# Optimization experiments

Hardware: AMD Instinct MI355X
Metric: run time of the kernel (lower is better)

## Reference

```python
import jax, jax.numpy as jnp
import numpy as np
import math

B, S, D = 2, 1024, 1024
H = 16
HD = D // H
E = 8
DFF = 4096
EPS = 1e-5


def _ln(x, g, b):
    m = jnp.mean(x, axis=-1, keepdims=True)
    v = jnp.mean((x - m) ** 2, axis=-1, keepdims=True)
    return (x - m) / jnp.sqrt(v + EPS) * g + b


def setup_inputs() -> dict:
    key = jax.random.key(0)
    ks = jax.random.split(key, 16)
    s = 0.02
    inp = {
        'src': jax.random.normal(ks[0], (B, S, D), jnp.float32),
        'qw': jax.random.normal(ks[1], (D, D), jnp.float32) * s,
        'kw': jax.random.normal(ks[2], (D, D), jnp.float32) * s,
        'vw': jax.random.normal(ks[3], (D, D), jnp.float32) * s,
        'ow': jax.random.normal(ks[4], (D, D), jnp.float32) * s,
        'gate_w': jax.random.normal(ks[5], (D, D), jnp.float32) * s,
        'gate_b': jax.random.normal(ks[6], (D,), jnp.float32) * s,
        'scale_w': jax.random.normal(ks[7], (H, HD), jnp.float32) * s,
        'n1_g': jnp.ones((D,), jnp.float32),
        'n1_b': jnp.zeros((D,), jnp.float32),
        'n2_g': jnp.ones((D,), jnp.float32),
        'n2_b': jnp.zeros((D,), jnp.float32),
        'moe_gate_w': jax.random.normal(ks[8], (D, E), jnp.float32) * s,
        'moe_gate_b': jnp.zeros((E,), jnp.float32),
        'w1': jax.random.normal(ks[9], (E, D, DFF), jnp.float32) * s,
        'b1': jnp.zeros((E, DFF), jnp.float32),
        'ln_g': jnp.ones((E, DFF), jnp.float32),
        'ln_b': jnp.zeros((E, DFF), jnp.float32),
        'w2': jax.random.normal(ks[10], (E, DFF, D), jnp.float32) * s,
        'b2': jnp.zeros((E, D), jnp.float32),
        'res_scale': jnp.ones((E,), jnp.float32),
    }
    return inp


def _forward(src, qw, kw, vw, ow, gate_w, gate_b, scale_w, n1_g, n1_b, n2_g, n2_b,
             moe_gate_w, moe_gate_b, w1, b1, ln_g, ln_b, w2, b2, res_scale):
    # ---- MemoAttention (non-flash path, eval: no dropout, no mask) ----
    q = (src @ qw).reshape(B, S, H, HD).transpose(0, 2, 1, 3)  # [B,H,S,HD]
    k = (src @ kw).reshape(B, S, H, HD).transpose(0, 2, 1, 3)
    v = (src @ vw).reshape(B, S, H, HD).transpose(0, 2, 1, 3)
    scores = jnp.einsum('bhqd,bhkd->bhqk', q, k) / math.sqrt(HD)
    # dynamic per-(head,query) scale gate
    scale = jax.nn.sigmoid(jnp.einsum('bhsd,hd->bhs', q, scale_w)) * 2.0
    scores = scores * scale[..., None]
    attn = jax.nn.softmax(scores, axis=-1)
    out = jnp.einsum('bhqk,bhkd->bhqd', attn, v)
    out = out.transpose(0, 2, 1, 3).reshape(B, S, D)
    gate = jax.nn.sigmoid(out @ gate_w + gate_b)
    attn_out = (out * gate) @ ow

    x = _ln(src + attn_out, n1_g, n1_b)

    # ---- MoE FFN (top-2 routing; eval: no gate noise; capacity never exceeded) ----
    xf = x.reshape(-1, D)                      # [T, D]
    T = xf.shape[0]
    logits = xf @ moe_gate_w + moe_gate_b      # [T, E]
    top_v, top_i = jax.lax.top_k(logits, 2)
    # NB: original sums BOTH top-k softmax weights per token (== 1.0), and the
    wsum = jnp.sum(jax.nn.softmax(top_v, axis=-1), axis=-1)   # [T] (== 1)
    e_sel = jnp.max(top_i, axis=-1)                           # [T]
    # dense per-expert FFN on all tokens, then per-token select (masked compute)
    h = jnp.einsum('td,edf->etf', xf, w1) + b1[:, None, :]    # [E,T,DFF]
    h = _ln(h, ln_g[:, None, :], ln_b[:, None, :])
    h = jax.nn.gelu(h, approximate=False)                     # torch nn.GELU (erf)
    y = jnp.einsum('etf,efd->etd', h, w2) + b2[:, None, :]    # [E,T,D]
    y = y * res_scale[:, None, None] + xf[None]
    sel = jnp.take_along_axis(y, e_sel[None, :, None], axis=0)[0]  # [T,D]
    moe_out = (sel * wsum[:, None]).reshape(B, S, D)

    return _ln(x + moe_out, n2_g, n2_b)


def reference(src, qw, kw, vw, ow, gate_w, gate_b, scale_w, n1_g, n1_b, n2_g, n2_b,
              moe_gate_w, moe_gate_b, w1, b1, ln_g, ln_b, w2, b2, res_scale):
    return _forward(src, qw, kw, vw, ow, gate_w, gate_b, scale_w, n1_g, n1_b,
                    n2_g, n2_b, moe_gate_w, moe_gate_b, w1, b1, ln_g, ln_b,
                    w2, b2, res_scale)
```

## Files before the change

kernel.cpp:

```cpp
#include <hip/hip_runtime.h>
#include <math.h>

#define TOK    2048
#define DMODEL 1024
#define NHEAD  16
#define HDIM   64
#define NEXP   8
#define DFFN   4096

typedef unsigned short u16;
typedef __attribute__((ext_vector_type(8))) short short8;
typedef __attribute__((ext_vector_type(4))) float floatx4;

__device__ __forceinline__ float sigmoidf_(float x) { return 1.f / (1.f + expf(-x)); }

__device__ __forceinline__ u16 f2bf(float f) {
  union { float f; unsigned u; } v; v.f = f;
  unsigned r = v.u + 0x7FFFu + ((v.u >> 16) & 1u);
  return (u16)(r >> 16);
}
__device__ __forceinline__ float bf2f(u16 h) {
  union { unsigned u; float f; } v; v.u = ((unsigned)h) << 16; return v.f;
}

__device__ __forceinline__ void gload16(const void* g, void* l) {
  __builtin_amdgcn_global_load_lds((const __attribute__((address_space(1))) void*)g,
                                   (__attribute__((address_space(3))) void*)l, 16, 0, 0);
}

__device__ __forceinline__ float blockReduceSum256(float val) {
  __shared__ float ws_[4];
  #pragma unroll
  for (int off = 32; off; off >>= 1) val += __shfl_down(val, off);
  int lane = threadIdx.x & 63, w = threadIdx.x >> 6;
  if (lane == 0) ws_[w] = val;
  __syncthreads();
  float r = ws_[0] + ws_[1] + ws_[2] + ws_[3];
  __syncthreads();
  return r;
}

__global__ __launch_bounds__(256) void split_kernel(
    const float* __restrict__ X, u16* __restrict__ Hi, u16* __restrict__ Lo) {
  const int i = blockIdx.x * 256 + threadIdx.x;
  const float4 v = ((const float4*)X)[i];
  const float f[4] = {v.x, v.y, v.z, v.w};
  union { u16 s[4]; uint2 u; } h, l;
  #pragma unroll
  for (int j = 0; j < 4; ++j) {
    h.s[j] = f2bf(f[j]);
    l.s[j] = f2bf(f[j] - bf2f(h.s[j]));
  }
  ((uint2*)Hi)[i] = h.u;
  ((uint2*)Lo)[i] = l.u;
}

template<bool LO>
__global__ __launch_bounds__(256) void wt_conv_kernel(
    const float* __restrict__ W, u16* __restrict__ Whi, u16* __restrict__ Wlo,
    int K, int N) {
  const size_t z = blockIdx.z;
  W   += z * (size_t)K * N;
  Whi += z * (size_t)K * N;
  if (LO) Wlo += z * (size_t)K * N;
  __shared__ float tile[32][33];
  const int n0 = blockIdx.x * 32, k0 = blockIdx.y * 32;
  const int r = threadIdx.x >> 3, c4 = (threadIdx.x & 7) * 4;
  const float4 v = *(const float4*)&W[(size_t)(k0 + r) * N + n0 + c4];
  tile[r][c4+0] = v.x; tile[r][c4+1] = v.y; tile[r][c4+2] = v.z; tile[r][c4+3] = v.w;
  __syncthreads();
  union { u16 s[4]; uint2 u; } h, l;
  #pragma unroll
  for (int j = 0; j < 4; ++j) {
    const float f = tile[c4 + j][r];
    h.s[j] = f2bf(f);
    if (LO) l.s[j] = f2bf(f - bf2f(h.s[j]));
  }
  *(uint2*)&Whi[(size_t)(n0 + r) * K + k0 + c4] = h.u;
  if (LO) *(uint2*)&Wlo[(size_t)(n0 + r) * K + k0 + c4] = l.u;
}

template<int EPI>
__global__ __launch_bounds__(256, 2) void gemm_split_kernel(
    const u16* __restrict__ Ahi, const u16* __restrict__ Alo,
    const u16* __restrict__ Whi, const u16* __restrict__ Wlo,
    const float* __restrict__ bias, const float* __restrict__ mul,
    float* __restrict__ Cf, u16* __restrict__ Chi, u16* __restrict__ Clo,
    int M, int N, int K) {
  __shared__ u16 Ah[128*64], Al[128*64], Bh[128*64], Bl[128*64];
  const int tid = threadIdx.x;
  const int lane = tid & 63, wave = tid >> 6;
  const int row0 = blockIdx.y * 128, col0 = blockIdx.x * 128;
  const int wm = (wave & 1) * 64, wn = (wave >> 1) * 64;
  const int mr = tid >> 3;
  const int ksrc = (tid & 7) ^ ((tid >> 3) & 7);
  const floatx4 zero = {0.f, 0.f, 0.f, 0.f};
  floatx4 acc[4][4];
  #pragma unroll
  for (int i = 0; i < 4; ++i)
    #pragma unroll
    for (int j = 0; j < 4; ++j) acc[i][j] = zero;

  for (int k0 = 0; k0 < K; k0 += 64) {
    __syncthreads();
    #pragma unroll
    for (int p = 0; p < 4; ++p) {
      const int m = p * 32 + mr;
      const size_t ga = (size_t)(row0 + m) * K + (k0 + ksrc * 8);
      const size_t gb = (size_t)(col0 + m) * K + (k0 + ksrc * 8);
      const size_t off = (size_t)(p * 256 + wave * 64) * 16;
      gload16(Ahi + ga, (char*)Ah + off);
      gload16(Alo + ga, (char*)Al + off);
      gload16(Whi + gb, (char*)Bh + off);
      gload16(Wlo + gb, (char*)Bl + off);
    }
    __syncthreads();
    #pragma unroll
    for (int kk = 0; kk < 2; ++kk) {
      short8 ah[4], al[4], bh[4], bl[4];
      #pragma unroll
      for (int i = 0; i < 4; ++i) {
        const int ml = wm + i * 16 + (lane & 15);
        const int cm = (kk * 4 + (lane >> 4)) ^ (ml & 7);
        ah[i] = *(const short8*)&Ah[ml * 64 + cm * 8];
        al[i] = *(const short8*)&Al[ml * 64 + cm * 8];
        const int nl = wn + i * 16 + (lane & 15);
        const int cn = (kk * 4 + (lane >> 4)) ^ (nl & 7);
        bh[i] = *(const short8*)&Bh[nl * 64 + cn * 8];
        bl[i] = *(const short8*)&Bl[nl * 64 + cn * 8];
      }
      #pragma unroll
      for (int i = 0; i < 4; ++i)
        #pragma unroll
        for (int j = 0; j < 4; ++j) {
          acc[i][j] = __builtin_amdgcn_mfma_f32_16x16x32_bf16(ah[i], bh[j], acc[i][j], 0, 0, 0);
          acc[i][j] = __builtin_amdgcn_mfma_f32_16x16x32_bf16(al[i], bh[j], acc[i][j], 0, 0, 0);
          acc[i][j] = __builtin_amdgcn_mfma_f32_16x16x32_bf16(ah[i], bl[j], acc[i][j], 0, 0, 0);
        }
    }
  }
  const int cl = lane & 15, quad = lane >> 4;
  #pragma unroll
  for (int i = 0; i < 4; ++i)
    #pragma unroll
    for (int j = 0; j < 4; ++j) {
      const int col = col0 + wn + j * 16 + cl;
      #pragma unroll
      for (int r = 0; r < 4; ++r) {
        const int row = row0 + wm + i * 16 + quad * 4 + r;
        const float v = acc[i][j][r];
        if (EPI == 0) {
          Cf[(size_t)row * N + col] = v;
        } else if (EPI == 1) {
          const float s = sigmoidf_(v + bias[col]);
          const float g = s * mul[(size_t)row * N + col];
          const u16 hh = f2bf(g);
          Chi[(size_t)row * N + col] = hh;
          Clo[(size_t)row * N + col] = f2bf(g - bf2f(hh));
        } else {
          const u16 hh = f2bf(v);
          Chi[(size_t)row * N + col] = hh;
          Clo[(size_t)row * N + col] = f2bf(v - bf2f(hh));
        }
      }
    }
}

template<int EPI>
__global__ __launch_bounds__(256, 2) void gemm_moe_kernel(
    const u16* __restrict__ A, const u16* __restrict__ Wt,
    const float* __restrict__ bias, const float* __restrict__ rsc,
    const float* __restrict__ Xres,
    const int* __restrict__ perm, const int* __restrict__ offs,
    const int* __restrict__ counts,
    u16* __restrict__ Hout, float* __restrict__ Yout,
    int N, int K, int e_base) {
  const int ez = blockIdx.z, e = e_base + ez;
  const int ne = counts[e];
  const int tm = blockIdx.y;
  if (tm * 128 >= ne) return;
  __shared__ u16 As_[128*64], Bs_[128*64];
  __shared__ int toks[128];
  const int tid = threadIdx.x;
  if (tid < 128) {
    const int idx = tm * 128 + tid;
    toks[tid] = perm[offs[e] + (idx < ne ? idx : 0)];
  }
  __syncthreads();
  const int lane = tid & 63, wave = tid >> 6;
  const int wm = (wave & 1) * 64, wn = (wave >> 1) * 64;
  const int mr = tid >> 3;
  const int ksrc = (tid & 7) ^ ((tid >> 3) & 7);
  size_t abase[4];
  #pragma unroll
  for (int p = 0; p < 4; ++p) abase[p] = (size_t)toks[p * 32 + mr] * K;
  const u16* We = Wt + (size_t)ez * N * K;
  const int col0 = blockIdx.x * 128;
  const floatx4 zero = {0.f, 0.f, 0.f, 0.f};
  floatx4 acc[4][4];
  #pragma unroll
  for (int i = 0; i < 4; ++i)
    #pragma unroll
    for (int j = 0; j < 4; ++j) acc[i][j] = zero;

  for (int k0 = 0; k0 < K; k0 += 64) {
    __syncthreads();
    #pragma unroll
    for (int p = 0; p < 4; ++p) {
      const size_t off = (size_t)(p * 256 + wave * 64) * 16;
      gload16(A + abase[p] + (k0 + ksrc * 8), (char*)As_ + off);
      gload16(We + (size_t)(col0 + p * 32 + mr) * K + (k0 + ksrc * 8), (char*)Bs_ + off);
    }
    __syncthreads();
    #pragma unroll
    for (int kk = 0; kk < 2; ++kk) {
      short8 a[4], b[4];
      #pragma unroll
      for (int i = 0; i < 4; ++i) {
        const int ml = wm + i * 16 + (lane & 15);
        const int cm = (kk * 4 + (lane >> 4)) ^ (ml & 7);
        a[i] = *(const short8*)&As_[ml * 64 + cm * 8];
        const int nl = wn + i * 16 + (lane & 15);
        const int cn = (kk * 4 + (lane >> 4)) ^ (nl & 7);
        b[i] = *(const short8*)&Bs_[nl * 64 + cn * 8];
      }
      #pragma unroll
      for (int i = 0; i < 4; ++i)
        #pragma unroll
        for (int j = 0; j < 4; ++j)
          acc[i][j] = __builtin_amdgcn_mfma_f32_16x16x32_bf16(a[i], b[j], acc[i][j], 0, 0, 0);
    }
  }
  const int cl = lane & 15, quad = lane >> 4;
  const float rse = (EPI == 1) ? rsc[e] : 0.f;
  #pragma unroll
  for (int i = 0; i < 4; ++i)
    #pragma unroll
    for (int j = 0; j < 4; ++j) {
      const int col = col0 + wn + j * 16 + cl;
      #pragma unroll
      for (int r = 0; r < 4; ++r) {
        const int rl = wm + i * 16 + quad * 4 + r;
        if (tm * 128 + rl < ne) {
          const int tok = toks[rl];
          const float v = acc[i][j][r] + bias[(size_t)e * N + col];
          if (EPI == 0) Hout[(size_t)tok * N + col] = f2bf(v);
          else          Yout[(size_t)tok * N + col] = v * rse + Xres[(size_t)tok * N + col];
        }
      }
    }
}

__global__ __launch_bounds__(256) void vt_trans_kernel(
    const u16* __restrict__ QKh, const u16* __restrict__ QKl,
    u16* __restrict__ Vth, u16* __restrict__ Vtl) {
  const int tt = blockIdx.x;
  const int bh = blockIdx.y;
  const int b = bh >> 4, h = bh & 15;
  __shared__ u16 th[64][72], tl[64][72];
  const int t = threadIdx.x;
  const int r = t >> 3, c8 = (t & 7) * 8;
  #pragma unroll
  for (int p = 0; p < 2; ++p) {
    const int tok = p * 32 + r;
    const size_t g = ((size_t)b * 1024 + tt * 64 + tok) * 3072 + 2048 + h * 64 + c8;
    *(uint4*)&th[tok][c8] = *(const uint4*)&QKh[g];
    *(uint4*)&tl[tok][c8] = *(const uint4*)&QKl[g];
  }
  __syncthreads();
  #pragma unroll
  for (int p = 0; p < 2; ++p) {
    const int d = p * 32 + r;
    union { u16 s[8]; uint4 u; } oh, ol;
    #pragma unroll
    for (int j = 0; j < 8; ++j) { oh.s[j] = th[c8 + j][d]; ol.s[j] = tl[c8 + j][d]; }
    const size_t g = ((size_t)bh * 64 + d) * 1024 + tt * 64 + c8;
    *(uint4*)&Vth[g] = oh.u;
    *(uint4*)&Vtl[g] = ol.u;
  }
}

__global__ __launch_bounds__(256, 2) void attn_mfma_kernel(
    const u16* __restrict__ QKh, const u16* __restrict__ QKl,
    const u16* __restrict__ Vth, const u16* __restrict__ Vtl,
    const float* __restrict__ scale_w,
    float* __restrict__ AOf, u16* __restrict__ AOh, u16* __restrict__ AOl) {
  const int qt = blockIdx.x, h = blockIdx.y, b = blockIdx.z;
  __shared__ u16 Kh[64*64], Kl[64*64], Vh[64*64], Vl[64*64];
  __shared__ u16 Ph[4][16*72], Pl[4][16*72];
  const int tid = threadIdx.x, lane = tid & 63, wave = tid >> 6;
  const int i15 = lane & 15, quad = lane >> 4;
  const floatx4 zero = {0.f, 0.f, 0.f, 0.f};

  short8 qh[2], ql[2];
  const size_t qrow = ((size_t)b * 1024 + qt * 64 + wave * 16 + i15) * 3072 + h * 64;
  #pragma unroll
  for (int kk = 0; kk < 2; ++kk) {
    qh[kk] = *(const short8*)&QKh[qrow + kk * 32 + quad * 8];
    ql[kk] = *(const short8*)&QKl[qrow + kk * 32 + quad * 8];
  }
  float dot = 0.f;
  #pragma unroll
  for (int kk = 0; kk < 2; ++kk)
    #pragma unroll
    for (int j = 0; j < 8; ++j) {
      const float sw = scale_w[h * 64 + kk * 32 + quad * 8 + j];
      dot += (bf2f((u16)qh[kk][j]) + bf2f((u16)ql[kk][j])) * sw;
    }
  dot += __shfl_xor(dot, 16);
  dot += __shfl_xor(dot, 32);
  const float g = 2.f * sigmoidf_(dot) * 0.125f;
  float stot[4];
  #pragma unroll
  for (int r = 0; r < 4; ++r) stot[r] = __shfl(g, (lane >> 4) * 4 + r);

  float m_r[4], l_r[4];
  floatx4 Of[4];
  #pragma unroll
  for (int r = 0; r < 4; ++r) { m_r[r] = -1e30f; l_r[r] = 0.f; }
  #pragma unroll
  for (int f = 0; f < 4; ++f) Of[f] = zero;
  u16* PhW = Ph[wave];
  u16* PlW = Pl[wave];

  const int sr = tid >> 3, sc = ((tid & 7) ^ ((tid >> 3) & 7)) * 8;
  for (int kt = 0; kt < 16; ++kt) {
    __syncthreads();
    #pragma unroll
    for (int p = 0; p < 2; ++p) {
      const int row = p * 32 + sr;
      const size_t off = (size_t)(p * 256 + wave * 64) * 16;
      const size_t kg = ((size_t)b * 1024 + kt * 64 + row) * 3072 + 1024 + h * 64 + sc;
      gload16(QKh + kg, (char*)Kh + off);
      gload16(QKl + kg, (char*)Kl + off);
      const size_t vg = ((size_t)(b * 16 + h) * 64 + row) * 1024 + kt * 64 + sc;
      gload16(Vth + vg, (char*)Vh + off);
      gload16(Vtl + vg, (char*)Vl + off);
    }
    __syncthreads();
    float pm[4][4];
    #pragma unroll
    for (int jn = 0; jn < 4; ++jn) {
      floatx4 a = zero;
      #pragma unroll
      for (int kk = 0; kk < 2; ++kk) {
        const int n = jn * 16 + i15;
        const int ch = ((kk * 4 + quad) ^ (n & 7)) * 8;
        const short8 bh = *(const short8*)&Kh[n * 64 + ch];
        const short8 bl = *(const short8*)&Kl[n * 64 + ch];
        a = __builtin_amdgcn_mfma_f32_16x16x32_bf16(qh[kk], bh, a, 0, 0, 0);
        a = __builtin_amdgcn_mfma_f32_16x16x32_bf16(ql[kk], bh, a, 0, 0, 0);
        a = __builtin_amdgcn_mfma_f32_16x16x32_bf16(qh[kk], bl, a, 0, 0, 0);
      }
      #pragma unroll
      for (int r = 0; r < 4; ++r) pm[jn][r] = a[r] * stot[r];
    }
    float alpha[4];
    #pragma unroll
    for (int r = 0; r < 4; ++r) {
      float mx = fmaxf(fmaxf(pm[0][r], pm[1][r]), fmaxf(pm[2][r], pm[3][r]));
      mx = fmaxf(mx, __shfl_xor(mx, 1));
      mx = fmaxf(mx, __shfl_xor(mx, 2));
      mx = fmaxf(mx, __shfl_xor(mx, 4));
      mx = fmaxf(mx, __shfl_xor(mx, 8));
      const float mn = fmaxf(m_r[r], mx);
      alpha[r] = expf(m_r[r] - mn);
      m_r[r] = mn;
      float rs = 0.f;
      #pragma unroll
      for (int jn = 0; jn < 4; ++jn) { pm[jn][r] = expf(pm[jn][r] - mn); rs += pm[jn][r]; }
      rs += __shfl_xor(rs, 1);
      rs += __shfl_xor(rs, 2);
      rs += __shfl_xor(rs, 4);
      rs += __shfl_xor(rs, 8);
      l_r[r] = l_r[r] * alpha[r] + rs;
    }
    #pragma unroll
    for (int f = 0; f < 4; ++f)
      #pragma unroll
      for (int r = 0; r < 4; ++r) Of[f][r] *= alpha[r];
    #pragma unroll
    for (int jn = 0; jn < 4; ++jn)
      #pragma unroll
      for (int r = 0; r < 4; ++r) {
        const int a = (quad * 4 + r) * 72 + jn * 16 + i15;
        const u16 hh = f2bf(pm[jn][r]);
        PhW[a] = hh;
        PlW[a] = f2bf(pm[jn][r] - bf2f(hh));
      }
    #pragma unroll
    for (int kk = 0; kk < 2; ++kk) {
      const short8 pah = *(const short8*)&PhW[i15 * 72 + kk * 32 + quad * 8];
      const short8 pal = *(const short8*)&PlW[i15 * 72 + kk * 32 + quad * 8];
      #pragma unroll
      for (int f = 0; f < 4; ++f) {
        const int d = f * 16 + i15;
        const int ch = ((kk * 4 + quad) ^ (d & 7)) * 8;
        const short8 vbh = *(const short8*)&Vh[d * 64 + ch];
        const short8 vbl = *(const short8*)&Vl[d * 64 + ch];
        Of[f] = __builtin_amdgcn_mfma_f32_16x16x32_bf16(pah, vbh, Of[f], 0, 0, 0);
        Of[f] = __builtin_amdgcn_mfma_f32_16x16x32_bf16(pal, vbh, Of[f], 0, 0, 0);
        Of[f] = __builtin_amdgcn_mfma_f32_16x16x32_bf16(pah, vbl, Of[f], 0, 0, 0);
      }
    }
  }
  float inv[4];
  #pragma unroll
  for (int r = 0; r < 4; ++r) inv[r] = 1.f / l_r[r];
  #pragma unroll
  for (int f = 0; f < 4; ++f)
    #pragma unroll
    for (int r = 0; r < 4; ++r) {
      const size_t row = (size_t)b * 1024 + qt * 64 + wave * 16 + quad * 4 + r;
      const int col = h * 64 + f * 16 + i15;
      const float val = Of[f][r] * inv[r];
      AOf[row * 1024 + col] = val;
      const u16 hh = f2bf(val);
      AOh[row * 1024 + col] = hh;
      AOl[row * 1024 + col] = f2bf(val - bf2f(hh));
    }
}

template<bool BF>
__global__ __launch_bounds__(256) void ln_add_kernel(
    const float* __restrict__ A, const float* __restrict__ Bp,
    const float* __restrict__ g, const float* __restrict__ beta,
    float* __restrict__ outf, u16* __restrict__ outh) {
  int t = blockIdx.x, tid = threadIdx.x;
  const float* a = A + (size_t)t * DMODEL;
  const float* b = Bp + (size_t)t * DMODEL;
  float v[4]; float s = 0.f;
  #pragma unroll
  for (int i = 0; i < 4; ++i) { int d = tid + i*256; v[i] = a[d] + b[d]; s += v[i]; }
  s = blockReduceSum256(s);
  float mean = s * (1.f/1024.f);
  float q = 0.f;
  #pragma unroll
  for (int i = 0; i < 4; ++i) { float df = v[i]-mean; q += df*df; }
  q = blockReduceSum256(q);
  float rstd = rsqrtf(q*(1.f/1024.f) + 1e-5f);
  #pragma unroll
  for (int i = 0; i < 4; ++i) {
    int d = tid + i*256;
    float val = (v[i]-mean)*rstd*g[d] + beta[d];
    outf[(size_t)t*DMODEL + d] = val;
    if (BF) outh[(size_t)t*DMODEL + d] = f2bf(val);
  }
}

__global__ __launch_bounds__(256) void moe_gate_kernel(
    const float* __restrict__ X, const float* __restrict__ gw,
    const float* __restrict__ gb, int* __restrict__ e_sel) {
  int wave = threadIdx.x >> 6, lane = threadIdx.x & 63;
  int token = blockIdx.x * 4 + wave;
  const float* x = X + (size_t)token * DMODEL;
  float acc[NEXP] = {};
  for (int d = lane; d < DMODEL; d += 64) {
    float xv = x[d];
    const float* gr = gw + (size_t)d * NEXP;
    #pragma unroll
    for (int e = 0; e < NEXP; ++e) acc[e] += xv * gr[e];
  }
  #pragma unroll
  for (int e = 0; e < NEXP; ++e) {
    #pragma unroll
    for (int off = 32; off; off >>= 1) acc[e] += __shfl_down(acc[e], off);
  }
  if (lane == 0) {
    float lg[NEXP];
    #pragma unroll
    for (int e = 0; e < NEXP; ++e) lg[e] = acc[e] + gb[e];
    int i1 = 0;
    for (int e = 1; e < NEXP; ++e) if (lg[e] > lg[i1]) i1 = e;
    int i2 = -1;
    for (int e = 0; e < NEXP; ++e) {
      if (e == i1) continue;
      if (i2 < 0 || lg[e] > lg[i2]) i2 = e;
    }
    e_sel[token] = (i1 > i2) ? i1 : i2;
  }
}

__global__ __launch_bounds__(256) void moe_group_kernel(
    const int* __restrict__ e_sel, int* __restrict__ perm,
    int* __restrict__ g_offs, int* __restrict__ g_counts) {
  __shared__ int cnt[NEXP], offs[NEXP], cur[NEXP];
  int tid = threadIdx.x;
  if (tid < NEXP) cnt[tid] = 0;
  __syncthreads();
  for (int t = tid; t < TOK; t += 256) atomicAdd(&cnt[e_sel[t]], 1);
  __syncthreads();
  if (tid == 0) {
    int run = 0;
    for (int e = 0; e < NEXP; ++e) { offs[e] = run; cur[e] = run; run += cnt[e]; }
  }
  __syncthreads();
  if (tid < NEXP) { g_offs[tid] = offs[tid]; g_counts[tid] = cnt[tid]; }
  for (int t = tid; t < TOK; t += 256) {
    int pos = atomicAdd(&cur[e_sel[t]], 1);
    perm[pos] = t;
  }
}

__global__ __launch_bounds__(256) void moe_ln_gelu_kernel(
    u16* __restrict__ H, const float* __restrict__ ln_g,
    const float* __restrict__ ln_b, const int* __restrict__ e_sel) {
  int t = blockIdx.x, tid = threadIdx.x;
  int e = e_sel[t];
  u16* h = H + (size_t)t * DFFN;
  float v[16]; float s = 0.f;
  #pragma unroll
  for (int i = 0; i < 16; ++i) { v[i] = bf2f(h[tid + i*256]); s += v[i]; }
  s = blockReduceSum256(s);
  float mean = s * (1.f/4096.f);
  float q = 0.f;
  #pragma unroll
  for (int i = 0; i < 16; ++i) { float df = v[i]-mean; q += df*df; }
  q = blockReduceSum256(q);
  float rstd = rsqrtf(q*(1.f/4096.f) + 1e-5f);
  const float* gg = ln_g + (size_t)e * DFFN;
  const float* bb = ln_b + (size_t)e * DFFN;
  #pragma unroll
  for (int i = 0; i < 16; ++i) {
    int d = tid + i*256;
    float x = (v[i]-mean)*rstd*gg[d] + bb[d];
    h[d] = f2bf(0.5f * x * (1.f + erff(x * 0.7071067811865475f)));
  }
}

extern "C" void kernel_launch(void* const* d_in, const int* in_sizes, int n_in,
                              void* d_out, int out_size, void* d_ws, size_t ws_size,
                              hipStream_t stream) {
  (void)in_sizes; (void)n_in; (void)out_size; (void)ws_size;
  const float* src    = (const float*)d_in[0];
  const float* qw     = (const float*)d_in[1];
  const float* kw     = (const float*)d_in[2];
  const float* vw     = (const float*)d_in[3];
  const float* ow     = (const float*)d_in[4];
  const float* gate_w = (const float*)d_in[5];
  const float* gate_b = (const float*)d_in[6];
  const float* scale_w= (const float*)d_in[7];
  const float* n1_g   = (const float*)d_in[8];
  const float* n1_b   = (const float*)d_in[9];
  const float* n2_g   = (const float*)d_in[10];
  const float* n2_b   = (const float*)d_in[11];
  const float* mgw    = (const float*)d_in[12];
  const float* mgb    = (const float*)d_in[13];
  const float* w1     = (const float*)d_in[14];
  const float* b1     = (const float*)d_in[15];
  const float* ln_g   = (const float*)d_in[16];
  const float* ln_b   = (const float*)d_in[17];
  const float* w2     = (const float*)d_in[18];
  const float* b2     = (const float*)d_in[19];
  const float* rs     = (const float*)d_in[20];

  char* ws = (char*)d_ws;
  const size_t MB = 1024 * 1024;
  u16*   qkv_hi = (u16*)(ws + 0*MB);
  u16*   qkv_lo = (u16*)(ws + 12*MB);
  u16*   Wt3_hi = (u16*)(ws + 24*MB);
  u16*   Wt3_lo = (u16*)(ws + 30*MB);
  u16*   Vt_hi  = (u16*)(ws + 36*MB);
  u16*   Vt_lo  = (u16*)(ws + 40*MB);
  u16*   src_hi = (u16*)(ws + 44*MB);
  u16*   src_lo = (u16*)(ws + 48*MB);
  float* ao     = (float*)(ws + 44*MB);
  u16*   ao_hi  = (u16*)(ws + 52*MB);
  u16*   ao_lo  = (u16*)(ws + 56*MB);
  u16*   gb_hi  = (u16*)(ws + 60*MB);
  u16*   gb_lo  = (u16*)(ws + 64*MB);
  float* proj   = (float*)(ws + 0*MB);
  float* x      = (float*)(ws + 8*MB);
  u16*   x_hi   = (u16*)(ws + 16*MB);
  u16*   WtA    = (u16*)(ws + 24*MB);
  u16*   h      = (u16*)(ws + 56*MB);
  float* y      = (float*)(ws + 72*MB);
  int*   e_sel  = (int*)(ws + 80*MB);
  int*   perm   = e_sel + TOK;
  int*   offs   = perm + TOK;
  int*   cnts   = offs + NEXP;

  dim3 blk(256);
  split_kernel<<<2048, blk, 0, stream>>>(src, src_hi, src_lo);

  wt_conv_kernel<true><<<dim3(32,32,1), blk, 0, stream>>>(qw, Wt3_hi, Wt3_lo, DMODEL, DMODEL);
  wt_conv_kernel<true><<<dim3(32,32,1), blk, 0, stream>>>(kw, Wt3_hi + 1024*1024, Wt3_lo + 1024*1024, DMODEL, DMODEL);
  wt_conv_kernel<true><<<dim3(32,32,1), blk, 0, stream>>>(vw, Wt3_hi + 2048*1024, Wt3_lo + 2048*1024, DMODEL, DMODEL);
  gemm_split_kernel<2><<<dim3(24,16), blk, 0, stream>>>(src_hi, src_lo, Wt3_hi, Wt3_lo,
      nullptr, nullptr, nullptr, qkv_hi, qkv_lo, TOK, 3072, DMODEL);

  vt_trans_kernel<<<dim3(16,32), blk, 0, stream>>>(qkv_hi, qkv_lo, Vt_hi, Vt_lo);
  attn_mfma_kernel<<<dim3(16, NHEAD, 2), blk, 0, stream>>>(
      qkv_hi, qkv_lo, Vt_hi, Vt_lo, scale_w, ao, ao_hi, ao_lo);

  wt_conv_kernel<true><<<dim3(32,32,1), blk, 0, stream>>>(gate_w, Wt3_hi, Wt3_lo, DMODEL, DMODEL);
  gemm_split_kernel<1><<<dim3(8,16), blk, 0, stream>>>(ao_hi, ao_lo, Wt3_hi, Wt3_lo,
      gate_b, ao, nullptr, gb_hi, gb_lo, TOK, DMODEL, DMODEL);
  wt_conv_kernel<true><<<dim3(32,32,1), blk, 0, stream>>>(ow, Wt3_hi, Wt3_lo, DMODEL, DMODEL);
  gemm_split_kernel<0><<<dim3(8,16), blk, 0, stream>>>(gb_hi, gb_lo, Wt3_hi, Wt3_lo,
      nullptr, nullptr, proj, nullptr, nullptr, TOK, DMODEL, DMODEL);

  ln_add_kernel<true><<<TOK, blk, 0, stream>>>(src, proj, n1_g, n1_b, x, x_hi);

  moe_gate_kernel<<<TOK/4, blk, 0, stream>>>(x, mgw, mgb, e_sel);
  moe_group_kernel<<<1, blk, 0, stream>>>(e_sel, perm, offs, cnts);

  for (int c = 0; c < 2; ++c) {
    wt_conv_kernel<false><<<dim3(DFFN/32, DMODEL/32, 4), blk, 0, stream>>>(
        w1 + (size_t)c*4*DMODEL*DFFN, WtA, nullptr, DMODEL, DFFN);
    gemm_moe_kernel<0><<<dim3(DFFN/128, 16, 4), blk, 0, stream>>>(
        x_hi, WtA, b1, nullptr, nullptr, perm, offs, cnts, h, nullptr, DFFN, DMODEL, c*4);
  }
  moe_ln_gelu_kernel<<<TOK, blk, 0, stream>>>(h, ln_g, ln_b, e_sel);
  for (int c = 0; c < 2; ++c) {
    wt_conv_kernel<false><<<dim3(DMODEL/32, DFFN/32, 4), blk, 0, stream>>>(
        w2 + (size_t)c*4*DFFN*DMODEL, WtA, nullptr, DFFN, DMODEL);
    gemm_moe_kernel<1><<<dim3(DMODEL/128, 16, 4), blk, 0, stream>>>(
        h, WtA, b2, rs, x, perm, offs, cnts, nullptr, y, DMODEL, DFFN, c*4);
  }
  ln_add_kernel<false><<<TOK, blk, 0, stream>>>(x, y, n2_g, n2_b, (float*)d_out, nullptr);
}
```

Before: 808.5 us.

## Halve GEMM N-tiles, split-K the MoE down-projection, fuse bias/residual into final LN

Narrows the N tile from 128 to 64 in both the split-bf16 GEMM and the MoE grouped GEMM, doubling the block count and raising the occupancy hint, so these small grids fill more compute units. The second MoE GEMM now splits K into two halves written to separate fp32 partial buffers. A new final LayerNorm kernel sums the partials and applies the bias, residual scale and residual before normalizing. This trades more redundant A-tile loads and an extra partial-buffer round trip for better parallelism on grids that were sparse because each expert receives only a few tokens.

Result: faster. 714.6 us (-11.6%).

```diff
diff --git a/kernel.cpp b/kernel.cpp
--- a/kernel.cpp
+++ b/kernel.cpp
@@ -81,58 +81,64 @@
 }
 
 template<int EPI>
-__global__ __launch_bounds__(256, 2) void gemm_split_kernel(
+__global__ __launch_bounds__(256, 3) void gemm_split_kernel(
     const u16* __restrict__ Ahi, const u16* __restrict__ Alo,
     const u16* __restrict__ Whi, const u16* __restrict__ Wlo,
     const float* __restrict__ bias, const float* __restrict__ mul,
     float* __restrict__ Cf, u16* __restrict__ Chi, u16* __restrict__ Clo,
     int M, int N, int K) {
-  __shared__ u16 Ah[128*64], Al[128*64], Bh[128*64], Bl[128*64];
+  __shared__ u16 Ah[128*64], Al[128*64], Bh[64*64], Bl[64*64];
   const int tid = threadIdx.x;
   const int lane = tid & 63, wave = tid >> 6;
-  const int row0 = blockIdx.y * 128, col0 = blockIdx.x * 128;
-  const int wm = (wave & 1) * 64, wn = (wave >> 1) * 64;
+  const int row0 = blockIdx.y * 128, col0 = blockIdx.x * 64;
+  const int wm = (wave & 1) * 64, wn = (wave >> 1) * 32;
   const int mr = tid >> 3;
   const int ksrc = (tid & 7) ^ ((tid >> 3) & 7);
   const floatx4 zero = {0.f, 0.f, 0.f, 0.f};
-  floatx4 acc[4][4];
+  floatx4 acc[4][2];
   #pragma unroll
   for (int i = 0; i < 4; ++i)
     #pragma unroll
-    for (int j = 0; j < 4; ++j) acc[i][j] = zero;
+    for (int j = 0; j < 2; ++j) acc[i][j] = zero;
 
   for (int k0 = 0; k0 < K; k0 += 64) {
     __syncthreads();
     #pragma unroll
     for (int p = 0; p < 4; ++p) {
-      const int m = p * 32 + mr;
-      const size_t ga = (size_t)(row0 + m) * K + (k0 + ksrc * 8);
-      const size_t gb = (size_t)(col0 + m) * K + (k0 + ksrc * 8);
+      const size_t ga = (size_t)(row0 + p * 32 + mr) * K + (k0 + ksrc * 8);
       const size_t off = (size_t)(p * 256 + wave * 64) * 16;
       gload16(Ahi + ga, (char*)Ah + off);
       gload16(Alo + ga, (char*)Al + off);
+    }
+    #pragma unroll
+    for (int p = 0; p < 2; ++p) {
+      const size_t gb = (size_t)(col0 + p * 32 + mr) * K + (k0 + ksrc * 8);
+      const size_t off = (size_t)(p * 256 + wave * 64) * 16;
       gload16(Whi + gb, (char*)Bh + off);
       gload16(Wlo + gb, (char*)Bl + off);
     }
     __syncthreads();
     #pragma unroll
     for (int kk = 0; kk < 2; ++kk) {
-      short8 ah[4], al[4], bh[4], bl[4];
+      short8 ah[4], al[4], bh[2], bl[2];
       #pragma unroll
       for (int i = 0; i < 4; ++i) {
         const int ml = wm + i * 16 + (lane & 15);
         const int cm = (kk * 4 + (lane >> 4)) ^ (ml & 7);
         ah[i] = *(const short8*)&Ah[ml * 64 + cm * 8];
         al[i] = *(const short8*)&Al[ml * 64 + cm * 8];
-        const int nl = wn + i * 16 + (lane & 15);
+      }
+      #pragma unroll
+      for (int j = 0; j < 2; ++j) {
+        const int nl = wn + j * 16 + (lane & 15);
         const int cn = (kk * 4 + (lane >> 4)) ^ (nl & 7);
-        bh[i] = *(const short8*)&Bh[nl * 64 + cn * 8];
-        bl[i] = *(const short8*)&Bl[nl * 64 + cn * 8];
+        bh[j] = *(const short8*)&Bh[nl * 64 + cn * 8];
+        bl[j] = *(const short8*)&Bl[nl * 64 + cn * 8];
       }
       #pragma unroll
       for (int i = 0; i < 4; ++i)
         #pragma unroll
-        for (int j = 0; j < 4; ++j) {
+        for (int j = 0; j < 2; ++j) {
           acc[i][j] = __builtin_amdgcn_mfma_f32_16x16x32_bf16(ah[i], bh[j], acc[i][j], 0, 0, 0);
           acc[i][j] = __builtin_amdgcn_mfma_f32_16x16x32_bf16(al[i], bh[j], acc[i][j], 0, 0, 0);
           acc[i][j] = __builtin_amdgcn_mfma_f32_16x16x32_bf16(ah[i], bl[j], acc[i][j], 0, 0, 0);
@@ -143,7 +149,7 @@
   #pragma unroll
   for (int i = 0; i < 4; ++i)
     #pragma unroll
-    for (int j = 0; j < 4; ++j) {
+    for (int j = 0; j < 2; ++j) {
       const int col = col0 + wn + j * 16 + cl;
       #pragma unroll
       for (int r = 0; r < 4; ++r) {
@@ -167,19 +173,23 @@
 }
 
 template<int EPI>
-__global__ __launch_bounds__(256, 2) void gemm_moe_kernel(
+__global__ __launch_bounds__(256, 4) void gemm_moe_kernel(
     const u16* __restrict__ A, const u16* __restrict__ Wt,
-    const float* __restrict__ bias, const float* __restrict__ rsc,
-    const float* __restrict__ Xres,
+    const float* __restrict__ bias,
     const int* __restrict__ perm, const int* __restrict__ offs,
     const int* __restrict__ counts,
-    u16* __restrict__ Hout, float* __restrict__ Yout,
+    u16* __restrict__ Hout, float* __restrict__ P0, float* __restrict__ P1,
     int N, int K, int e_base) {
-  const int ez = blockIdx.z, e = e_base + ez;
+  const int z = blockIdx.z;
+  const int ez = (EPI == 0) ? z : (z & 3);
+  const int ks = (EPI == 0) ? 0 : (z >> 2);
+  const int e = e_base + ez;
   const int ne = counts[e];
   const int tm = blockIdx.y;
   if (tm * 128 >= ne) return;
-  __shared__ u16 As_[128*64], Bs_[128*64];
+  const int kbeg = (EPI == 0) ? 0 : ks * (K >> 1);
+  const int kend = (EPI == 0) ? K : kbeg + (K >> 1);
+  __shared__ u16 As_[128*64], Bs_[64*64];
   __shared__ int toks[128];
   const int tid = threadIdx.x;
   if (tid < 128) {
@@ -188,64 +198,72 @@
   }
   __syncthreads();
   const int lane = tid & 63, wave = tid >> 6;
-  const int wm = (wave & 1) * 64, wn = (wave >> 1) * 64;
+  const int wm = (wave & 1) * 64, wn = (wave >> 1) * 32;
   const int mr = tid >> 3;
   const int ksrc = (tid & 7) ^ ((tid >> 3) & 7);
   size_t abase[4];
   #pragma unroll
   for (int p = 0; p < 4; ++p) abase[p] = (size_t)toks[p * 32 + mr] * K;
   const u16* We = Wt + (size_t)ez * N * K;
-  const int col0 = blockIdx.x * 128;
+  const int col0 = blockIdx.x * 64;
   const floatx4 zero = {0.f, 0.f, 0.f, 0.f};
-  floatx4 acc[4][4];
+  floatx4 acc[4][2];
   #pragma unroll
   for (int i = 0; i < 4; ++i)
     #pragma unroll
-    for (int j = 0; j < 4; ++j) acc[i][j] = zero;
-
-  for (int k0 = 0; k0 < K; k0 += 64) {
+    for (int j = 0; j < 2; ++j) acc[i][j] = zero;
+
+  for (int k0 = kbeg; k0 < kend; k0 += 64) {
     __syncthreads();
     #pragma unroll
     for (int p = 0; p < 4; ++p) {
       const size_t off = (size_t)(p * 256 + wave * 64) * 16;
       gload16(A + abase[p] + (k0 + ksrc * 8), (char*)As_ + off);
+    }
+    #pragma unroll
+    for (int p = 0; p < 2; ++p) {
+      const size_t off = (size_t)(p * 256 + wave * 64) * 16;
       gload16(We + (size_t)(col0 + p * 32 + mr) * K + (k0 + ksrc * 8), (char*)Bs_ + off);
     }
     __syncthreads();
     #pragma unroll
     for (int kk = 0; kk < 2; ++kk) {
-      short8 a[4], b[4];
+      short8 a[4], b[2];
       #pragma unroll
       for (int i = 0; i < 4; ++i) {
         const int ml = wm + i * 16 + (lane & 15);
         const int cm = (kk * 4 + (lane >> 4)) ^ (ml & 7);
         a[i] = *(const short8*)&As_[ml * 64 + cm * 8];
-        const int nl = wn + i * 16 + (lane & 15);
+      }
+      #pragma unroll
+      for (int j = 0; j < 2; ++j) {
+        const int nl = wn + j * 16 + (lane & 15);
         const int cn = (kk * 4 + (lane >> 4)) ^ (nl & 7);
-        b[i] = *(const short8*)&Bs_[nl * 64 + cn * 8];
+        b[j] = *(const short8*)&Bs_[nl * 64 + cn * 8];
       }
       #pragma unroll
       for (int i = 0; i < 4; ++i)
         #pragma unroll
-        for (int j = 0; j < 4; ++j)
+        for (int j = 0; j < 2; ++j)
           acc[i][j] = __builtin_amdgcn_mfma_f32_16x16x32_bf16(a[i], b[j], acc[i][j], 0, 0, 0);
     }
   }
   const int cl = lane & 15, quad = lane >> 4;
-  const float rse = (EPI == 1) ? rsc[e] : 0.f;
+  float* Pp = (EPI == 1) ? (ks ? P1 : P0) : nullptr;
   #pragma unroll
   for (int i = 0; i < 4; ++i)
     #pragma unroll
-    for (int j = 0; j < 4; ++j) {
+    for (int j = 0; j < 2; ++j) {
       const int col = col0 + wn + j * 16 + cl;
       #pragma unroll
       for (int r = 0; r < 4; ++r) {
         const int rl = wm + i * 16 + quad * 4 + r;
         if (tm * 128 + rl < ne) {
           const int tok = toks[rl];
-          const float v = acc[i][j][r] + bias[(size_t)e * N + col];
-          if (EPI == 0) Hout[(size_t)tok * N + col] = f2bf(v);
-          else          Yout[(size_t)tok * N + col] = v * rse + Xres[(size_t)tok * N + col];
+          if (EPI == 0)
+            Hout[(size_t)tok * N + col] = f2bf(acc[i][j][r] + bias[(size_t)e * N + col]);
+          else
+            Pp[(size_t)tok * N + col] = acc[i][j][r];
         }
       }
     }
@@ -445,6 +463,40 @@
     float val = (v[i]-mean)*rstd*g[d] + beta[d];
     outf[(size_t)t*DMODEL + d] = val;
     if (BF) outh[(size_t)t*DMODEL + d] = f2bf(val);
+  }
+}
+
+__global__ __launch_bounds__(256) void ln_final_kernel(
+    const float* __restrict__ X, const float* __restrict__ P0,
+    const float* __restrict__ P1, const float* __restrict__ B2,
+    const float* __restrict__ rsv, const int* __restrict__ e_sel,
+    const float* __restrict__ g, const float* __restrict__ beta,
+    float* __restrict__ out) {
+  int t = blockIdx.x, tid = threadIdx.x;
+  const int e = e_sel[t];
+  const float rse = rsv[e];
+  const float* b2e = B2 + (size_t)e * DMODEL;
+  float v[4]; float s = 0.f;
+  #pragma unroll
+  for (int i = 0; i < 4; ++i) {
+    int d = tid + i*256;
+    const size_t idx = (size_t)t * DMODEL + d;
+    const float xv = X[idx];
+    const float yv = (P0[idx] + P1[idx] + b2e[d]) * rse + xv;
+    v[i] = xv + yv;
+    s += v[i];
+  }
+  s = blockReduceSum256(s);
+  float mean = s * (1.f/1024.f);
+  float q = 0.f;
+  #pragma unroll
+  for (int i = 0; i < 4; ++i) { float df = v[i]-mean; q += df*df; }
+  q = blockReduceSum256(q);
+  float rstd = rsqrtf(q*(1.f/1024.f) + 1e-5f);
+  #pragma unroll
+  for (int i = 0; i < 4; ++i) {
+    int d = tid + i*256;
+    out[(size_t)t*DMODEL + d] = (v[i]-mean)*rstd*g[d] + beta[d];
   }
 }
 
@@ -574,7 +626,8 @@
   u16*   x_hi   = (u16*)(ws + 16*MB);
   u16*   WtA    = (u16*)(ws + 24*MB);
   u16*   h      = (u16*)(ws + 56*MB);
-  float* y      = (float*)(ws + 72*MB);
+  float* p0     = (float*)(ws + 0*MB);
+  float* p1     = (float*)(ws + 72*MB);
   int*   e_sel  = (int*)(ws + 80*MB);
   int*   perm   = e_sel + TOK;
   int*   offs   = perm + TOK;
@@ -586,7 +639,7 @@
   wt_conv_kernel<true><<<dim3(32,32,1), blk, 0, stream>>>(qw, Wt3_hi, Wt3_lo, DMODEL, DMODEL);
   wt_conv_kernel<true><<<dim3(32,32,1), blk, 0, stream>>>(kw, Wt3_hi + 1024*1024, Wt3_lo + 1024*1024, DMODEL, DMODEL);
   wt_conv_kernel<true><<<dim3(32,32,1), blk, 0, stream>>>(vw, Wt3_hi + 2048*1024, Wt3_lo + 2048*1024, DMODEL, DMODEL);
-  gemm_split_kernel<2><<<dim3(24,16), blk, 0, stream>>>(src_hi, src_lo, Wt3_hi, Wt3_lo,
+  gemm_split_kernel<2><<<dim3(48,16), blk, 0, stream>>>(src_hi, src_lo, Wt3_hi, Wt3_lo,
       nullptr, nullptr, nullptr, qkv_hi, qkv_lo, TOK, 3072, DMODEL);
 
   vt_trans_kernel<<<dim3(16,32), blk, 0, stream>>>(qkv_hi, qkv_lo, Vt_hi, Vt_lo);
@@ -594,10 +647,10 @@
       qkv_hi, qkv_lo, Vt_hi, Vt_lo, scale_w, ao, ao_hi, ao_lo);
 
   wt_conv_kernel<true><<<dim3(32,32,1), blk, 0, stream>>>(gate_w, Wt3_hi, Wt3_lo, DMODEL, DMODEL);
-  gemm_split_kernel<1><<<dim3(8,16), blk, 0, stream>>>(ao_hi, ao_lo, Wt3_hi, Wt3_lo,
+  gemm_split_kernel<1><<<dim3(16,16), blk, 0, stream>>>(ao_hi, ao_lo, Wt3_hi, Wt3_lo,
       gate_b, ao, nullptr, gb_hi, gb_lo, TOK, DMODEL, DMODEL);
   wt_conv_kernel<true><<<dim3(32,32,1), blk, 0, stream>>>(ow, Wt3_hi, Wt3_lo, DMODEL, DMODEL);
-  gemm_split_kernel<0><<<dim3(8,16), blk, 0, stream>>>(gb_hi, gb_lo, Wt3_hi, Wt3_lo,
+  gemm_split_kernel<0><<<dim3(16,16), blk, 0, stream>>>(gb_hi, gb_lo, Wt3_hi, Wt3_lo,
       nullptr, nullptr, proj, nullptr, nullptr, TOK, DMODEL, DMODEL);
 
   ln_add_kernel<true><<<TOK, blk, 0, stream>>>(src, proj, n1_g, n1_b, x, x_hi);
@@ -608,15 +661,15 @@
   for (int c = 0; c < 2; ++c) {
     wt_conv_kernel<false><<<dim3(DFFN/32, DMODEL/32, 4), blk, 0, stream>>>(
         w1 + (size_t)c*4*DMODEL*DFFN, WtA, nullptr, DMODEL, DFFN);
-    gemm_moe_kernel<0><<<dim3(DFFN/128, 16, 4), blk, 0, stream>>>(
-        x_hi, WtA, b1, nullptr, nullptr, perm, offs, cnts, h, nullptr, DFFN, DMODEL, c*4);
+    gemm_moe_kernel<0><<<dim3(DFFN/64, 16, 4), blk, 0, stream>>>(
+        x_hi, WtA, b1, perm, offs, cnts, h, nullptr, nullptr, DFFN, DMODEL, c*4);
   }
   moe_ln_gelu_kernel<<<TOK, blk, 0, stream>>>(h, ln_g, ln_b, e_sel);
   for (int c = 0; c < 2; ++c) {
     wt_conv_kernel<false><<<dim3(DMODEL/32, DFFN/32, 4), blk, 0, stream>>>(
         w2 + (size_t)c*4*DFFN*DMODEL, WtA, nullptr, DFFN, DMODEL);
-    gemm_moe_kernel<1><<<dim3(DMODEL/128, 16, 4), blk, 0, stream>>>(
-        h, WtA, b2, rs, x, perm, offs, cnts, nullptr, y, DMODEL, DFFN, c*4);
-  }
-  ln_add_kernel<false><<<TOK, blk, 0, stream>>>(x, y, n2_g, n2_b, (float*)d_out, nullptr);
-}
+    gemm_moe_kernel<1><<<dim3(DMODEL/64, 16, 8), blk, 0, stream>>>(
+        h, WtA, nullptr, perm, offs, cnts, nullptr, p0, p1, DMODEL, DFFN, c*4);
+  }
+  ln_final_kernel<<<TOK, blk, 0, stream>>>(x, p0, p1, b2, rs, e_sel, n2_g, n2_b, (float*)d_out);
+}
```
